# Kernel optimization log

Measured on AMD Instinct MI355X. Metric: run time of the kernel, lower is better.

## Reference

```python
import jax, jax.numpy as jnp
import numpy as np

B, N, X, Y, W1, W2, D = 2, 6, 8, 8, 8, 8, 128
H, DH = 4, 32
L = X * Y          # number of windows
QT = N * W1 * W2   # tokens per window
EPS = 1e-5


def _ln(x, g, b):
    m = x.mean(-1, keepdims=True)
    v = ((x - m) ** 2).mean(-1, keepdims=True)
    return (x - m) * jax.lax.rsqrt(v + EPS) * g + b


def _win(t):
    # b n x y w1 w2 d -> b (x y) (n w1 w2) d
    return t.transpose(0, 2, 3, 1, 4, 5, 6).reshape(B, L, QT, D)


def setup_inputs() -> dict:
    key = jax.random.key(0)
    ks = jax.random.split(key, 12)
    s = 0.02
    inp = {
        'q': jax.random.normal(ks[0], (B, N, X, Y, W1, W2, D), jnp.float32),
        'k': jax.random.normal(ks[1], (B, N, X, Y, W1, W2, D), jnp.float32),
        'v': jax.random.normal(ks[2], (B, N, X, Y, W1, W2, D), jnp.float32),
        'skip': jax.random.normal(ks[3], (B, X, Y, W1, W2, D), jnp.float32),
        'gq': jnp.ones((D,), jnp.float32), 'betq': jnp.zeros((D,), jnp.float32),
        'gk': jnp.ones((D,), jnp.float32), 'betk': jnp.zeros((D,), jnp.float32),
        'gv': jnp.ones((D,), jnp.float32), 'betv': jnp.zeros((D,), jnp.float32),
        'wq': jax.random.normal(ks[4], (D, H * DH), jnp.float32) * s,
        'bq': jnp.zeros((H * DH,), jnp.float32),
        'wk': jax.random.normal(ks[5], (D, H * DH), jnp.float32) * s,
        'bk': jnp.zeros((H * DH,), jnp.float32),
        'wv': jax.random.normal(ks[6], (D, H * DH), jnp.float32) * s,
        'bv': jnp.zeros((H * DH,), jnp.float32),
        'wp': jax.random.normal(ks[7], (H * DH, D), jnp.float32) * s,
        'bp': jnp.zeros((D,), jnp.float32),
    }
    return inp


def reference(q, k, v, skip, gq, betq, gk, betk, gv, betv,
              wq, bq, wk, bk, wv, bv, wp, bp):
    scale = DH ** -0.5
    qw, kw, vw = _win(q), _win(k), _win(v)
    # LayerNorm + Linear QKV, split heads: (b, l, T, h, dh)
    qh = (_ln(qw, gq, betq) @ wq + bq).reshape(B, L, QT, H, DH)
    kh = (_ln(kw, gk, betk) @ wk + bk).reshape(B, L, QT, H, DH)
    vh = (_ln(vw, gv, betv) @ wv + bv).reshape(B, L, QT, H, DH)
    dot = scale * jnp.einsum('blqhd,blkhd->bhlqk', qh, kh)
    att = jax.nn.softmax(dot, axis=-1)
    a = jnp.einsum('bhlqk,blkhd->blqhd', att, vh).reshape(B, L, QT, H * DH)
    # b (x y) (n w1 w2) d -> b n x y w1 w2 d
    a = a.reshape(B, X, Y, N, W1, W2, H * DH).transpose(0, 3, 1, 2, 4, 5, 6)
    z = a @ wp + bp
    z = z.mean(1)  # average over views
    return z + skip
```

## Files before the change

### kernel.cpp

```cpp
#include <hip/hip_runtime.h>


typedef unsigned short u16;
typedef __bf16 bf16x8 __attribute__((ext_vector_type(8)));
typedef __bf16 bf16x4 __attribute__((ext_vector_type(4)));
typedef float  f32x16 __attribute__((ext_vector_type(16)));
typedef unsigned short u16x8 __attribute__((ext_vector_type(8)));
typedef unsigned short u16x4 __attribute__((ext_vector_type(4)));

union U8 { u16x8 u; bf16x8 b; u16x4 h[2]; };

#if __has_builtin(__builtin_amdgcn_exp2f)
#define EXP2(x) __builtin_amdgcn_exp2f(x)
#else
#define EXP2(x) exp2f(x)
#endif

__device__ __forceinline__ f32x16 mfma_bf16(bf16x8 a, bf16x8 b, f32x16 c){
  return __builtin_amdgcn_mfma_f32_32x32x16_bf16(a, b, c, 0, 0, 0);
}


__global__ __launch_bounds__(512) void k_prep(
    const float* __restrict__ wq, const float* __restrict__ bq,
    const float* __restrict__ gq, const float* __restrict__ betq,
    const float* __restrict__ wk, const float* __restrict__ bk,
    const float* __restrict__ gk, const float* __restrict__ betk,
    const float* __restrict__ wv, const float* __restrict__ bv,
    const float* __restrict__ gv, const float* __restrict__ betv,
    const float* __restrict__ wp,
    u16* __restrict__ wqT, u16* __restrict__ wkT, u16* __restrict__ wvT, u16* __restrict__ wpT,
    float* __restrict__ bq2, float* __restrict__ bk2, float* __restrict__ bv2,
    float* __restrict__ uq2, float* __restrict__ uk2, float* __restrict__ uv2)
{
  __shared__ float wls[128*129];
  __shared__ float gls[128], bls[128];
  __shared__ float redb[512], redu[512];
  const float ALPHA_Q = 0.17677669529663687f * 1.4426950408889634f;
  int wsel = blockIdx.x, tid = threadIdx.x;
  const float *w, *bb, *g, *bet; u16* wT; float *b2, *u2; float alpha;
  if (wsel == 0){ w=wq; bb=bq; g=gq; bet=betq; wT=wqT; b2=bq2; u2=uq2; alpha=ALPHA_Q; }
  else if (wsel == 1){ w=wk; bb=bk; g=gk; bet=betk; wT=wkT; b2=bk2; u2=uk2; alpha=1.f; }
  else if (wsel == 2){ w=wv; bb=bv; g=gv; bet=betv; wT=wvT; b2=bv2; u2=uv2; alpha=1.f; }
  else { w=wp; bb=nullptr; g=nullptr; bet=nullptr; wT=wpT; b2=nullptr; u2=nullptr; alpha=1.f; }

  if (tid < 128){
    gls[tid] = g ? g[tid] : 1.f;
    bls[tid] = bet ? bet[tid] : 0.f;
  }
  const float4* w4 = (const float4*)w;
  #pragma unroll
  for (int i = 0; i < 8; i++){
    int idx = tid + i*512;
    int row = idx >> 5, c4 = (idx & 31) * 4;
    float4 x = w4[idx];
    wls[row*129 + c4 + 0] = x.x;
    wls[row*129 + c4 + 1] = x.y;
    wls[row*129 + c4 + 2] = x.z;
    wls[row*129 + c4 + 3] = x.w;
  }
  __syncthreads();
  int n = tid >> 2, qp = tid & 3;
  float sb = 0.f, su = 0.f;
  alignas(16) __bf16 tmp[32];
  #pragma unroll
  for (int kk = 0; kk < 32; kk++){
    int k2 = qp*32 + kk;
    float wv_ = wls[k2*129 + n];
    float gv_ = gls[k2];
    sb += bls[k2] * wv_;
    su += gv_ * wv_;
    tmp[kk] = (__bf16)(wv_ * gv_ * alpha);
  }
  #pragma unroll
  for (int j = 0; j < 4; j++)
    *(bf16x8*)(wT + n*128 + qp*32 + j*8) = *(bf16x8*)&tmp[j*8];
  redb[tid] = sb; redu[tid] = su;
  __syncthreads();
  if (qp == 0 && bb){
    float s = bb[n] + redb[tid] + redb[tid+1] + redb[tid+2] + redb[tid+3];
    float u = redu[tid] + redu[tid+1] + redu[tid+2] + redu[tid+3];
    b2[n] = s * alpha;
    u2[n] = u * alpha;
  }
}

__global__ __launch_bounds__(256) void k_lnproj(
    const float* __restrict__ qg, const float* __restrict__ kg, const float* __restrict__ vg,
    const u16* __restrict__ wqT, const u16* __restrict__ wkT, const u16* __restrict__ wvT,
    const float* __restrict__ bq2, const float* __restrict__ bk2, const float* __restrict__ bv2,
    const float* __restrict__ uq2, const float* __restrict__ uk2, const float* __restrict__ uv2,
    u16* __restrict__ qh, u16* __restrict__ kh, u16* __restrict__ vh)
{
  __shared__ alignas(16) u16 Abf[64*136];
  __shared__ float s1s[64], s2s[64];
  int bid = blockIdx.x, tid = threadIdx.x;
  int which = bid % 3;
  int t = bid / 3;
  int n = t % 6, bl = t / 6;
  const float* src; const u16* wT; const float *b2, *u2; u16* dstb;
  if (which == 0){ src=qg; wT=wqT; b2=bq2; u2=uq2; dstb=qh; }
  else if (which == 1){ src=kg; wT=wkT; b2=bk2; u2=uk2; dstb=kh; }
  else { src=vg; wT=wvT; b2=bv2; u2=uv2; dstb=vh; }
  int b = bl >> 6, l = bl & 63;
  const float4* s4 = (const float4*)(src + (size_t)((b*6 + n)*64 + l)*64*128);
  int row = tid >> 2, j = tid & 3;
  float s1 = 0.f, s2 = 0.f;
  #pragma unroll
  for (int i = 0; i < 8; i++){
    float4 xv = s4[row*32 + i*4 + j];
    s1 += xv.x + xv.y + xv.z + xv.w;
    s2 += xv.x*xv.x + xv.y*xv.y + xv.z*xv.z + xv.w*xv.w;
    bf16x4 pk;
    pk[0] = (__bf16)xv.x; pk[1] = (__bf16)xv.y;
    pk[2] = (__bf16)xv.z; pk[3] = (__bf16)xv.w;
    *(bf16x4*)&Abf[row*136 + (i*4 + j)*4] = pk;
  }
  s1 += __shfl_xor(s1, 1, 64); s1 += __shfl_xor(s1, 2, 64);
  s2 += __shfl_xor(s2, 1, 64); s2 += __shfl_xor(s2, 2, 64);
  if (j == 0){
    float m = s1 * (1.f/128.f);
    float r = rsqrtf(s2 * (1.f/128.f) - m*m + 1e-5f);
    s1s[row] = r;
    s2s[row] = r * m;
  }
  __syncthreads();
  int wave = tid >> 6, lane = tid & 63, lm = lane & 31, lh = lane >> 5;
  bf16x8 bfr[8];
  const u16* wrow = wT + (32*wave + lm)*128 + lh*8;
  #pragma unroll
  for (int ks = 0; ks < 8; ks++) bfr[ks] = *(const bf16x8*)(wrow + ks*16);
  f32x16 acc0, acc1;
  #pragma unroll
  for (int r = 0; r < 16; r++){ acc0[r]=0.f; acc1[r]=0.f; }
  #pragma unroll
  for (int ks = 0; ks < 8; ks++){
    bf16x8 a0 = *(const bf16x8*)&Abf[lm*136       + ks*16 + lh*8];
    bf16x8 a1 = *(const bf16x8*)&Abf[(32+lm)*136  + ks*16 + lh*8];
    acc0 = mfma_bf16(a0, bfr[ks], acc0);
    acc1 = mfma_bf16(a1, bfr[ks], acc1);
  }
  int col = 32*wave + lm;
  float u2c = u2[col], bc = b2[col];
  u16* dst = dstb + ((size_t)(bl*4 + wave)*384 + n*64)*32 + lm;
  #pragma unroll
  for (int r = 0; r < 16; r++){
    int row0 = (r&3) + 8*(r>>2) + 4*lh;
    float y0 = s1s[row0]     * acc0[r] - s2s[row0]     * u2c + bc;
    float y1 = s1s[row0+32]  * acc1[r] - s2s[row0+32]  * u2c + bc;
    *(__bf16*)&dst[(size_t)row0*32]      = (__bf16)y0;
    *(__bf16*)&dst[(size_t)(32+row0)*32] = (__bf16)y1;
  }
}

__global__ __launch_bounds__(384) void k_attn(
    const u16* __restrict__ qh, const u16* __restrict__ kh, const u16* __restrict__ vh,
    u16* __restrict__ abar)
{
  __shared__ alignas(16) u16 vts[32*408];
  __shared__ float abar_s[64*32];
  int bid = blockIdx.x, tid = threadIdx.x;
  int h = bid & 3, bl = bid >> 2;
  const u16* qb = qh + (size_t)bid * (384*32);
  const u16* kb = kh + (size_t)bid * (384*32);
  const u16* vb = vh + (size_t)bid * (384*32);

  int wave = tid >> 6, lane = tid & 63, lm = lane & 31, lh = lane >> 5;
  int n = wave;

  const u16* qbase = qb + (size_t)(n*64 + lm)*32 + lh*8;
  bf16x8 qfA0 = *(const bf16x8*)(qbase);
  bf16x8 qfA1 = *(const bf16x8*)(qbase + 16);
  bf16x8 qfB0 = *(const bf16x8*)(qbase + 32*32);
  bf16x8 qfB1 = *(const bf16x8*)(qbase + 32*32 + 16);

  #pragma unroll
  for (int i = 0; i < 4; i++){
    int c = tid + i*384;
    int key = c >> 2, part = c & 3;
    int u = key & 31, tt = key >> 5;
    int a = u >> 2;
    int anew = (a & 4) | ((a & 1) << 1) | ((a >> 1) & 1);
    int pos = tt*32 + anew*4 + (u & 3);
    u16x8 vv = *(const u16x8*)(vb + key*32 + part*8);
    #pragma unroll
    for (int jj = 0; jj < 8; jj++) vts[(part*8 + jj)*408 + pos] = vv[jj];
  }
  for (int idx = tid; idx < 2048; idx += 384) abar_s[idx] = 0.f;
  __syncthreads();

  const u16* vrow = &vts[lm*408 + 8*lh];
  const u16* krow = kb + lm*32 + lh*8;

  f32x16 oA, oB;
  #pragma unroll
  for (int r = 0; r < 16; r++){ oA[r] = 0.f; oB[r] = 0.f; }
  float sleA = 0.f, sleB = 0.f;

  #pragma unroll
  for (int kt = 0; kt < 12; kt++){
    bf16x8 kf0 = *(const bf16x8*)(krow + kt*(32*32));
    bf16x8 kf1 = *(const bf16x8*)(krow + kt*(32*32) + 16);
    f32x16 sa, sb_;
    #pragma unroll
    for (int r = 0; r < 16; r++){ sa[r] = 0.f; sb_[r] = 0.f; }
    sa  = mfma_bf16(kf0, qfA0, sa);
    sb_ = mfma_bf16(kf0, qfB0, sb_);
    sa  = mfma_bf16(kf1, qfA1, sa);
    sb_ = mfma_bf16(kf1, qfB1, sb_);
    U8 v0, v1;
    v0.u = *(const u16x8*)(vrow + kt*32);
    v1.u = *(const u16x8*)(vrow + kt*32 + 16);
    U8 pA0, pA1, pB0, pB1;
    #pragma unroll
    for (int r = 0; r < 8; r++){
      float eA0 = EXP2(sa[r]);
      float eA1 = EXP2(sa[r+8]);
      float eB0 = EXP2(sb_[r]);
      float eB1 = EXP2(sb_[r+8]);
      sleA += eA0 + eA1;
      sleB += eB0 + eB1;
      pA0.b[r] = (__bf16)eA0;
      pA1.b[r] = (__bf16)eA1;
      pB0.b[r] = (__bf16)eB0;
      pB1.b[r] = (__bf16)eB1;
    }
    oA = mfma_bf16(pA0.b, v0.b, oA);
    oB = mfma_bf16(pB0.b, v0.b, oB);
    oA = mfma_bf16(pA1.b, v1.b, oA);
    oB = mfma_bf16(pB1.b, v1.b, oB);
  }

  sleA += __shfl_xor(sleA, 32, 64);
  sleB += __shfl_xor(sleB, 32, 64);
  float invA = (1.f/6.f) / sleA;
  float invB = (1.f/6.f) / sleB;

  #pragma unroll
  for (int r = 0; r < 16; r++){
    int q_l = (r&3) + 8*(r>>2) + 4*lh;
    float a = oA[r] * __shfl(invA, q_l, 64);
    float b = oB[r] * __shfl(invB, q_l, 64);
    atomicAdd(&abar_s[q_l*32 + lm], a);
    atomicAdd(&abar_s[(32 + q_l)*32 + lm], b);
  }
  __syncthreads();
  u16* ob = abar + (size_t)(bl*64)*128 + h*32;
  for (int idx = tid; idx < 2048; idx += 384){
    int w12 = idx >> 5, dh = idx & 31;
    *(__bf16*)&ob[(size_t)w12*128 + dh] = (__bf16)abar_s[idx];
  }
}

__global__ __launch_bounds__(256) void k_out(
    const u16* __restrict__ abar, const u16* __restrict__ wpT,
    const float* __restrict__ bp, const float* __restrict__ skip,
    float* __restrict__ out)
{
  __shared__ alignas(16) u16 Als[64*136];
  int tid = threadIdx.x;
  int R0 = blockIdx.x * 64;
  #pragma unroll
  for (int i = 0; i < 4; i++){
    int c = tid + i*256;
    int row = c >> 4, part = c & 15;
    *(u16x8*)&Als[row*136 + part*8] = *(const u16x8*)(abar + (size_t)(R0+row)*128 + part*8);
  }
  __syncthreads();
  int wave = tid >> 6, lane = tid & 63, lm = lane & 31, lh = lane >> 5;
  bf16x8 bfr[8];
  const u16* wrow = wpT + (32*wave + lm)*128 + lh*8;
  #pragma unroll
  for (int ks = 0; ks < 8; ks++) bfr[ks] = *(const bf16x8*)(wrow + ks*16);
  f32x16 acc0, acc1;
  #pragma unroll
  for (int r = 0; r < 16; r++){ acc0[r]=0.f; acc1[r]=0.f; }
  #pragma unroll
  for (int ks = 0; ks < 8; ks++){
    bf16x8 a0 = *(const bf16x8*)&Als[lm*136      + ks*16 + lh*8];
    bf16x8 a1 = *(const bf16x8*)&Als[(32+lm)*136 + ks*16 + lh*8];
    acc0 = mfma_bf16(a0, bfr[ks], acc0);
    acc1 = mfma_bf16(a1, bfr[ks], acc1);
  }
  float bias = bp[32*wave + lm];
  #pragma unroll
  for (int r = 0; r < 16; r++){
    int row0 = (r&3) + 8*(r>>2) + 4*lh;
    size_t f0 = (size_t)(R0 + row0)*128 + 32*wave + lm;
    out[f0] = acc0[r] + bias + skip[f0];
    size_t f1 = (size_t)(R0 + 32 + row0)*128 + 32*wave + lm;
    out[f1] = acc1[r] + bias + skip[f1];
  }
}

extern "C" void kernel_launch(void* const* d_in, const int* in_sizes, int n_in,
                              void* d_out, int out_size, void* d_ws, size_t ws_size,
                              hipStream_t stream)
{
  const float* q    = (const float*)d_in[0];
  const float* k    = (const float*)d_in[1];
  const float* v    = (const float*)d_in[2];
  const float* skip = (const float*)d_in[3];
  const float* gq   = (const float*)d_in[4];
  const float* betq = (const float*)d_in[5];
  const float* gk   = (const float*)d_in[6];
  const float* betk = (const float*)d_in[7];
  const float* gv   = (const float*)d_in[8];
  const float* betv = (const float*)d_in[9];
  const float* wq   = (const float*)d_in[10];
  const float* bq   = (const float*)d_in[11];
  const float* wk   = (const float*)d_in[12];
  const float* bk   = (const float*)d_in[13];
  const float* wv   = (const float*)d_in[14];
  const float* bv   = (const float*)d_in[15];
  const float* wp   = (const float*)d_in[16];
  const float* bp   = (const float*)d_in[17];
  float* out = (float*)d_out;

  char* ws = (char*)d_ws;
  u16* wqT = (u16*)ws;
  u16* wkT = wqT + 16384;
  u16* wvT = wkT + 16384;
  u16* wpT = wvT + 16384;
  float* bq2 = (float*)(ws + 131072);
  float* bk2 = bq2 + 128;
  float* bv2 = bk2 + 128;
  float* uq2 = bv2 + 128;
  float* uk2 = uq2 + 128;
  float* uv2 = uk2 + 128;
  u16* qh = (u16*)(ws + 134144);
  u16* kh = qh + 6291456;
  u16* vh = kh + 6291456;
  u16* abar = vh + 6291456;

  k_prep  <<<4,    512, 0, stream>>>(wq,bq,gq,betq, wk,bk,gk,betk, wv,bv,gv,betv, wp,
                                     wqT,wkT,wvT,wpT, bq2,bk2,bv2, uq2,uk2,uv2);
  k_lnproj<<<2304, 256, 0, stream>>>(q,k,v, wqT,wkT,wvT, bq2,bk2,bv2, uq2,uk2,uv2, qh,kh,vh);
  k_attn  <<<512,  384, 0, stream>>>(qh,kh,vh, abar);
  k_out   <<<128,  256, 0, stream>>>(abar, wpT, bp, skip, out);
}
```

Baseline: 208.9 us.

## Split attention work across 12 waves with K/V prefetch and MFMA priority

Doubles the attention block to 768 threads so each wave handles one 32-query half instead of two, halving per-wave accumulator registers and raising wave-level parallelism. It also software-pipelines the K and V fragment loads one key tile ahead and wraps the MFMA calls with s_setprio. The intent is to hide global-load and exp latency behind more resident waves. The costs are more LDS atomic contention on the shared accumulator and K reads duplicated across twice as many waves.

```diff
diff --git a/kernel.cpp b/kernel.cpp
--- a/kernel.cpp
+++ b/kernel.cpp
@@ -153,30 +153,28 @@
   }
 }
 
-__global__ __launch_bounds__(384) void k_attn(
+__global__ __launch_bounds__(768, 6) void k_attn(
     const u16* __restrict__ qh, const u16* __restrict__ kh, const u16* __restrict__ vh,
     u16* __restrict__ abar)
 {
   __shared__ alignas(16) u16 vts[32*408];
   __shared__ float abar_s[64*32];
   int bid = blockIdx.x, tid = threadIdx.x;
-  int h = bid & 3, bl = bid >> 2;
+  int bl = bid >> 2;
   const u16* qb = qh + (size_t)bid * (384*32);
   const u16* kb = kh + (size_t)bid * (384*32);
   const u16* vb = vh + (size_t)bid * (384*32);
 
   int wave = tid >> 6, lane = tid & 63, lm = lane & 31, lh = lane >> 5;
-  int n = wave;
-
-  const u16* qbase = qb + (size_t)(n*64 + lm)*32 + lh*8;
-  bf16x8 qfA0 = *(const bf16x8*)(qbase);
-  bf16x8 qfA1 = *(const bf16x8*)(qbase + 16);
-  bf16x8 qfB0 = *(const bf16x8*)(qbase + 32*32);
-  bf16x8 qfB1 = *(const bf16x8*)(qbase + 32*32 + 16);
-
-  #pragma unroll
-  for (int i = 0; i < 4; i++){
-    int c = tid + i*384;
+  int n = wave >> 1, g = wave & 1;
+
+  const u16* qbase = qb + (size_t)(n*64 + g*32 + lm)*32 + lh*8;
+  bf16x8 qf0 = *(const bf16x8*)(qbase);
+  bf16x8 qf1 = *(const bf16x8*)(qbase + 16);
+
+  #pragma unroll
+  for (int i = 0; i < 2; i++){
+    int c = tid + i*768;
     int key = c >> 2, part = c & 3;
     int u = key & 31, tt = key >> 5;
     int a = u >> 2;
@@ -186,67 +184,67 @@
     #pragma unroll
     for (int jj = 0; jj < 8; jj++) vts[(part*8 + jj)*408 + pos] = vv[jj];
   }
-  for (int idx = tid; idx < 2048; idx += 384) abar_s[idx] = 0.f;
+  for (int idx = tid; idx < 2048; idx += 768) abar_s[idx] = 0.f;
   __syncthreads();
 
   const u16* vrow = &vts[lm*408 + 8*lh];
   const u16* krow = kb + lm*32 + lh*8;
 
-  f32x16 oA, oB;
-  #pragma unroll
-  for (int r = 0; r < 16; r++){ oA[r] = 0.f; oB[r] = 0.f; }
-  float sleA = 0.f, sleB = 0.f;
+  f32x16 o;
+  #pragma unroll
+  for (int r = 0; r < 16; r++) o[r] = 0.f;
+  float sle = 0.f;
+
+  bf16x8 kf0 = *(const bf16x8*)(krow);
+  bf16x8 kf1 = *(const bf16x8*)(krow + 16);
+  U8 v0, v1;
+  v0.u = *(const u16x8*)(vrow);
+  v1.u = *(const u16x8*)(vrow + 16);
 
   #pragma unroll
   for (int kt = 0; kt < 12; kt++){
-    bf16x8 kf0 = *(const bf16x8*)(krow + kt*(32*32));
-    bf16x8 kf1 = *(const bf16x8*)(krow + kt*(32*32) + 16);
-    f32x16 sa, sb_;
+    bf16x8 nk0, nk1; U8 nv0, nv1;
+    if (kt < 11){
+      nk0 = *(const bf16x8*)(krow + (kt+1)*1024);
+      nk1 = *(const bf16x8*)(krow + (kt+1)*1024 + 16);
+      nv0.u = *(const u16x8*)(vrow + (kt+1)*32);
+      nv1.u = *(const u16x8*)(vrow + (kt+1)*32 + 16);
+    }
+    f32x16 s;
     #pragma unroll
-    for (int r = 0; r < 16; r++){ sa[r] = 0.f; sb_[r] = 0.f; }
-    sa  = mfma_bf16(kf0, qfA0, sa);
-    sb_ = mfma_bf16(kf0, qfB0, sb_);
-    sa  = mfma_bf16(kf1, qfA1, sa);
-    sb_ = mfma_bf16(kf1, qfB1, sb_);
-    U8 v0, v1;
-    v0.u = *(const u16x8*)(vrow + kt*32);
-    v1.u = *(const u16x8*)(vrow + kt*32 + 16);
-    U8 pA0, pA1, pB0, pB1;
+    for (int r = 0; r < 16; r++) s[r] = 0.f;
+    __builtin_amdgcn_s_setprio(1);
+    s = mfma_bf16(kf0, qf0, s);
+    s = mfma_bf16(kf1, qf1, s);
+    __builtin_amdgcn_s_setprio(0);
+    U8 p0, p1;
     #pragma unroll
     for (int r = 0; r < 8; r++){
-      float eA0 = EXP2(sa[r]);
-      float eA1 = EXP2(sa[r+8]);
-      float eB0 = EXP2(sb_[r]);
-      float eB1 = EXP2(sb_[r+8]);
-      sleA += eA0 + eA1;
-      sleB += eB0 + eB1;
-      pA0.b[r] = (__bf16)eA0;
-      pA1.b[r] = (__bf16)eA1;
-      pB0.b[r] = (__bf16)eB0;
-      pB1.b[r] = (__bf16)eB1;
+      float e0 = EXP2(s[r]);
+      float e1 = EXP2(s[r+8]);
+      sle += e0 + e1;
+      p0.b[r] = (__bf16)e0;
+      p1.b[r] = (__bf16)e1;
     }
-    oA = mfma_bf16(pA0.b, v0.b, oA);
-    oB = mfma_bf16(pB0.b, v0.b, oB);
-    oA = mfma_bf16(pA1.b, v1.b, oA);
-    oB = mfma_bf16(pB1.b, v1.b, oB);
-  }
-
-  sleA += __shfl_xor(sleA, 32, 64);
-  sleB += __shfl_xor(sleB, 32, 64);
-  float invA = (1.f/6.f) / sleA;
-  float invB = (1.f/6.f) / sleB;
+    __builtin_amdgcn_s_setprio(1);
+    o = mfma_bf16(p0.b, v0.b, o);
+    o = mfma_bf16(p1.b, v1.b, o);
+    __builtin_amdgcn_s_setprio(0);
+    if (kt < 11){ kf0 = nk0; kf1 = nk1; v0 = nv0; v1 = nv1; }
+  }
+
+  sle += __shfl_xor(sle, 32, 64);
+  float inv = (1.f/6.f) / sle;
 
   #pragma unroll
   for (int r = 0; r < 16; r++){
     int q_l = (r&3) + 8*(r>>2) + 4*lh;
-    float a = oA[r] * __shfl(invA, q_l, 64);
-    float b = oB[r] * __shfl(invB, q_l, 64);
-    atomicAdd(&abar_s[q_l*32 + lm], a);
-    atomicAdd(&abar_s[(32 + q_l)*32 + lm], b);
-  }
-  __syncthreads();
-  u16* ob = abar + (size_t)(bl*64)*128 + h*32;
-  for (int idx = tid; idx < 2048; idx += 384){
+    float a = o[r] * __shfl(inv, q_l, 64);
+    atomicAdd(&abar_s[(g*32 + q_l)*32 + lm], a);
+  }
+  __syncthreads();
+  u16* ob = abar + (size_t)(bl*64)*128 + (bid & 3)*32;
+  for (int idx = tid; idx < 2048; idx += 768){
     int w12 = idx >> 5, dh = idx & 31;
     *(__bf16*)&ob[(size_t)w12*128 + dh] = (__bf16)abar_s[idx];
   }
@@ -336,6 +334,6 @@
   k_prep  <<<4,    512, 0, stream>>>(wq,bq,gq,betq, wk,bk,gk,betk, wv,bv,gv,betv, wp,
                                      wqT,wkT,wvT,wpT, bq2,bk2,bv2, uq2,uk2,uv2);
   k_lnproj<<<2304, 256, 0, stream>>>(q,k,v, wqT,wkT,wvT, bq2,bk2,bv2, uq2,uk2,uv2, qh,kh,vh);
-  k_attn  <<<512,  384, 0, stream>>>(qh,kh,vh, abar);
+  k_attn  <<<512,  768, 0, stream>>>(qh,kh,vh, abar);
   k_out   <<<128,  256, 0, stream>>>(abar, wpT, bp, skip, out);
 }
```

Result: slower. 216.7 us (+3.7%).
